# Performance work log

Hardware: AMD Instinct MI355X
Metric: run time of the kernel (lower is better)

Reference implementation:

```python
import jax, jax.numpy as jnp
import numpy as np

SIDE = 32
N_NODES = SIDE * SIDE          # n_nodes = 1024
WIDTH = 128
IN_DIM = 128
T_DIM = 2
U_DIM = 1
BATCH = 8
MSG_STEPS = int(np.sqrt(N_NODES))  # 32
LN_EPS = 1e-5


def _create_grid():
    # matches GEN.create_grid for t_dim == 2
    pos = np.array([[i / (SIDE - 1), j / (SIDE - 1)]
                    for i in range(SIDE) for j in range(SIDE)], dtype=np.float32)
    edges = []
    for i in range(1, SIDE):
        for j in range(1, SIDE):
            a = SIDE * i + j
            b = SIDE * (i - 1) + j
            c = SIDE * i + (j - 1)
            edges += [[a, b], [b, a], [c, a], [a, c]]
    edge_index = np.array(edges, dtype=np.int64).T  # [2, E]
    return pos, edge_index


def setup_inputs() -> dict:
    key = jax.random.key(0)
    ks = jax.random.split(key, 16)
    node_pos_np, edge_index_np = _create_grid()

    def lin(k, fan_in, fan_out):
        kw, kb = jax.random.split(k)
        bound = 1.0 / np.sqrt(fan_in)
        W = jax.random.uniform(kw, (fan_in, fan_out), jnp.float32, -bound, bound)
        b = jax.random.uniform(kb, (fan_out,), jnp.float32, -bound, bound)
        return W, b

    We1, be1 = lin(ks[0], IN_DIM, WIDTH)
    We2, be2 = lin(ks[1], WIDTH, WIDTH)
    We3, be3 = lin(ks[2], WIDTH, WIDTH)
    Wg, bg = lin(ks[3], WIDTH + T_DIM, WIDTH)
    Wd1, bd1 = lin(ks[4], WIDTH + T_DIM, WIDTH)
    Wd2, bd2 = lin(ks[5], WIDTH, WIDTH)
    Wd3, bd3 = lin(ks[6], WIDTH, U_DIM)

    return {
        'X1': jax.random.uniform(ks[7], (BATCH, IN_DIM + T_DIM), jnp.float32),
        'node_pos': jnp.asarray(node_pos_np),
        'edge_index': jnp.asarray(edge_index_np),
        'We1': We1, 'be1': be1, 'We2': We2, 'be2': be2, 'We3': We3, 'be3': be3,
        'Wg': Wg, 'bg': bg,
        'gamma': jnp.ones((WIDTH,), jnp.float32),
        'beta': jnp.zeros((WIDTH,), jnp.float32),
        'Wd1': Wd1, 'bd1': bd1, 'Wd2': Wd2, 'bd2': bd2, 'Wd3': Wd3, 'bd3': bd3,
    }


def _gen_forward(X1, node_pos, edge_index, We1, be1, We2, be2, We3, be3,
                 Wg, bg, gamma, beta, Wd1, bd1, Wd2, bd2, Wd3, bd3):
    s, t = X1[:, :-T_DIM], X1[:, -T_DIM:]

    # encoder MLP: Linear-ReLU-Linear-ReLU-Linear
    h = jax.nn.relu(s @ We1 + be1)
    h = jax.nn.relu(h @ We2 + be2)
    enc = h @ We3 + be3                                   # [B, W]

    # per-sample graph construction: softmax over node distance to origin
    # (identical for every sample), node_features = weight @ enc[i][None,:]
    d0 = jnp.sqrt(jnp.sum(node_pos ** 2, axis=1, keepdims=True))  # [N,1]
    w0 = jax.nn.softmax(-d0, axis=0)                              # [N,1]
    x = w0[None, :, :] * enc[:, None, :]                          # [B,N,W]

    # GCNConv normalization with added self-loops (symmetric norm)
    row, col = edge_index[0], edge_index[1]
    deg = jnp.ones((N_NODES,), x.dtype).at[col].add(1.0)
    dinv = deg ** -0.5
    enorm = dinv[row] * dinv[col]   # edge norm
    snorm = dinv * dinv             # self-loop norm
    posb = jnp.broadcast_to(node_pos[None], (x.shape[0], N_NODES, T_DIM))

    def step(xc, _):
        xin = jnp.concatenate([posb, xc], axis=-1)        # [B,N,W+2]
        xw = xin @ Wg                                     # [B,N,W]
        msgs = enorm[None, :, None] * xw[:, row, :]       # [B,E,W]
        agg = (snorm[None, :, None] * xw).at[:, col, :].add(msgs) + bg
        xn = xc + agg
        mu = jnp.mean(xn, axis=-1, keepdims=True)
        var = jnp.var(xn, axis=-1, keepdims=True)
        xn = (xn - mu) * jax.lax.rsqrt(var + LN_EPS) * gamma + beta
        return xn, None

    x, _ = jax.lax.scan(step, x, None, length=MSG_STEPS)  # [B,N,W]

    # readout: softmax over node distance to query point t
    dist = jnp.sqrt(jnp.sum((node_pos[None] - t[:, None, :]) ** 2,
                            axis=2, keepdims=True))       # [B,N,1]
    wt = jax.nn.softmax(-dist, axis=1)                    # [B,N,1]
    hidden = jnp.einsum('bnk,bnw->bw', wt, x)             # [B,W]
    hidden = jnp.concatenate([hidden, t], axis=1)

    h = jax.nn.relu(hidden @ Wd1 + bd1)
    h = jax.nn.relu(h @ Wd2 + bd2)
    y = (h @ Wd3 + bd3).squeeze()                         # [B] (u_dim == 1)
    return y


def reference(X1, node_pos, edge_index, We1, be1, We2, be2, We3, be3,
              Wg, bg, gamma, beta, Wd1, bd1, Wd2, bd2, Wd3, bd3):
    return _gen_forward(X1, node_pos, edge_index, We1, be1, We2, be2, We3, be3,
                        Wg, bg, gamma, beta, Wd1, bd1, Wd2, bd2, Wd3, bd3)
```

## Files before the change

### kernel.cpp

```cpp
#include <hip/hip_runtime.h>

#define NODES 1024
#define WD    128
#define NSTEPS 32
#define LNEPS 1e-5f

typedef __bf16 bf16x8 __attribute__((ext_vector_type(8)));
typedef float  f32x4  __attribute__((ext_vector_type(4)));
typedef int    i32x4  __attribute__((ext_vector_type(4)));

__device__ __forceinline__ f32x4 mfma16(i32x4 a, i32x4 b, f32x4 c) {
  return __builtin_amdgcn_mfma_f32_16x16x32_bf16(
      __builtin_bit_cast(bf16x8, a), __builtin_bit_cast(bf16x8, b), c, 0, 0, 0);
}

__device__ __forceinline__ unsigned short f2bf(float f) {
  union { float f; unsigned u; } v; v.f = f;
  unsigned r = v.u + 0x7FFF + ((v.u >> 16) & 1);
  return (unsigned short)(r >> 16);
}
__device__ __forceinline__ float bf2f(unsigned short h) {
  union { unsigned u; float f; } v; v.u = ((unsigned)h) << 16;
  return v.f;
}

__device__ __forceinline__ float dinv_of(int n) {
  const int i = n >> 5, j = n & 31;
  int cnt = 1;
  cnt += (i >= 1 && j >= 1) ? 1 : 0;
  cnt += (i <= 30 && j >= 1) ? 1 : 0;
  cnt += (i >= 1 && j >= 1) ? 1 : 0;
  cnt += (i >= 1 && j <= 30) ? 1 : 0;
  return 1.f / sqrtf((float)cnt);
}

__device__ void enc_layer(const float* __restrict__ W,
                          const float* __restrict__ bias,
                          const float* __restrict__ src, float* __restrict__ dst,
                          float* __restrict__ Wst, int tid, int b, int c,
                          bool relu_) {
  float acc = bias ? bias[c] : 0.f;
  for (int h = 0; h < 2; h++) {
    __syncthreads();
    for (int i = tid; i < 2048; i += 1024)
      ((float4*)Wst)[i] = ((const float4*)(W + h * 8192))[i];
    __syncthreads();
#pragma unroll 8
    for (int k = 0; k < 64; k++)
      acc += src[b * WD + 64 * h + k] * Wst[k * WD + c];
  }
  __syncthreads();
  dst[tid] = relu_ ? fmaxf(acc, 0.f) : acc;
}

__global__ __launch_bounds__(1024) void setup_kernel(
    const float* __restrict__ X1, const float* __restrict__ pos,
    const float* __restrict__ We1, const float* __restrict__ be1,
    const float* __restrict__ We2, const float* __restrict__ be2,
    const float* __restrict__ We3, const float* __restrict__ be3,
    const float* __restrict__ Wg,
    float* __restrict__ enc_out, float* __restrict__ E2,
    float* __restrict__ w0sum, int* __restrict__ Bpk) {
  __shared__ float Wst[64 * WD];
  __shared__ float ioA[1024];
  __shared__ float ioB[1024];
  const int tid = threadIdx.x;
  const int b = tid >> 7, c = tid & 127;
  ioA[tid] = X1[b * 130 + c];
  enc_layer(We1, be1, ioA, ioB, Wst, tid, b, c, true);
  enc_layer(We2, be2, ioB, ioA, Wst, tid, b, c, true);
  enc_layer(We3, be3, ioA, ioB, Wst, tid, b, c, false);
  enc_out[tid] = ioB[tid];
  const float* W2 = Wg + 2 * WD;
  {
    float acc = 0.f;
    for (int h = 0; h < 2; h++) {
      __syncthreads();
      for (int i = tid; i < 2048; i += 1024)
        ((float4*)Wst)[i] = ((const float4*)(W2 + h * 8192))[i];
      __syncthreads();
#pragma unroll 8
      for (int k = 0; k < 64; k++)
        acc += ioB[b * WD + 64 * h + k] * Wst[k * WD + c];
    }
    E2[tid] = acc;
  }
  __syncthreads();
  {
    const float px = pos[2 * tid], py = pos[2 * tid + 1];
    ioA[tid] = expf(-sqrtf(px * px + py * py));
  }
  __syncthreads();
  for (int s = 512; s > 0; s >>= 1) {
    if (tid < s) ioA[tid] += ioA[tid + s];
    __syncthreads();
  }
  if (tid == 0) w0sum[0] = ioA[0];
  if (tid < 512) {
    const int nt = tid >> 6, l = tid & 63;
    const int g8 = (l >> 4) << 3;
    const int n = 16 * nt + (l & 15);
    const int base = (nt * 64 + l) * 32;
#pragma unroll
    for (int kt = 0; kt < 4; kt++) {
#pragma unroll
      for (int d = 0; d < 4; d++) {
        const int k0 = 32 * kt + g8 + 2 * d;
        const float w0_ = W2[k0 * WD + n];
        const float w1_ = W2[(k0 + 1) * WD + n];
        const unsigned short h0 = f2bf(w0_), h1 = f2bf(w1_);
        const unsigned short l0 = f2bf(w0_ - bf2f(h0)), l1 = f2bf(w1_ - bf2f(h1));
        Bpk[base + kt * 4 + d] = (int)h0 | ((int)h1 << 16);
        Bpk[base + 16 + kt * 4 + d] = (int)l0 | ((int)l1 << 16);
      }
    }
  }
}

__global__ __launch_bounds__(256) void init_kernel(
    const float* __restrict__ pos, const float* __restrict__ Wg,
    const float* __restrict__ bg, const float* __restrict__ enc,
    const float* __restrict__ E2, const float* __restrict__ w0sum,
    float* __restrict__ X, float* __restrict__ XW0, float* __restrict__ Q) {
  const int tid = threadIdx.x;
  const int v0 = blockIdx.x * 4;
  const int lr = tid >> 3, cq = tid & 7, c0 = cq * 16;
  const int b = lr >> 2, nl = lr & 3, v = v0 + nl;
  const int grow = (b << 10) + v;
  const float px = pos[2 * v], py = pos[2 * v + 1];
  const float w0v = expf(-sqrtf(px * px + py * py)) / w0sum[0];
#pragma unroll
  for (int q4 = 0; q4 < 4; q4++) {
    const float4 e = *(const float4*)(enc + b * WD + c0 + 4 * q4);
    const float4 e2 = *(const float4*)(E2 + b * WD + c0 + 4 * q4);
    *(float4*)(X + (size_t)grow * WD + c0 + 4 * q4) =
        make_float4(w0v * e.x, w0v * e.y, w0v * e.z, w0v * e.w);
    *(float4*)(XW0 + (size_t)grow * WD + c0 + 4 * q4) =
        make_float4(w0v * e2.x, w0v * e2.y, w0v * e2.z, w0v * e2.w);
  }
  for (int i = tid; i < 512; i += 256) {
    const int vq = v0 + (i >> 7);
    const int cc = i & 127;
    const float dv = dinv_of(vq);
    const float dvv = dv * dv;
    const int iv = vq >> 5, jv = vq & 31;
    float cx = dvv * pos[2 * vq], cy = dvv * pos[2 * vq + 1];
    const bool ex[4] = {(iv >= 1) && (jv >= 1), (iv <= 30) && (jv >= 1),
                        (iv >= 1) && (jv >= 1), (iv >= 1) && (jv <= 30)};
    const int du[4] = {-32, 32, -1, 1};
#pragma unroll
    for (int e = 0; e < 4; e++) {
      if (ex[e]) {
        const int u = vq + du[e];
        const float w = dinv_of(u) * dv;
        cx += w * pos[2 * u];
        cy += w * pos[2 * u + 1];
      }
    }
    Q[vq * WD + cc] = bg[cc] + cx * Wg[cc] + cy * Wg[WD + cc];
  }
}

__global__ __launch_bounds__(256) void step_kernel(
    float* __restrict__ X, const float* __restrict__ XWin,
    float* __restrict__ XWout, const int* __restrict__ Bpk,
    const float* __restrict__ Q, const float* __restrict__ gamma,
    const float* __restrict__ beta, const int mode) {
  __shared__ int Ah[32 * 65];
  __shared__ int Al[32 * 65];
  const int tid = threadIdx.x;
  const int v0 = blockIdx.x * 4;

  const int lr = tid >> 3, cq = tid & 7, c0 = cq * 16;
  const int b = lr >> 2, nl = lr & 3, v = v0 + nl;
  const int grow = (b << 10) + v;
  const float dv = dinv_of(v);
  const float dvv = dv * dv;
  const int iv = v >> 5, jv = v & 31;
  const bool ex[4] = {(iv >= 1) && (jv >= 1), (iv <= 30) && (jv >= 1),
                      (iv >= 1) && (jv >= 1), (iv >= 1) && (jv <= 30)};
  const int du[4] = {-32, 32, -1, 1};

  float y[16];
  {
    const float* xr = X + (size_t)grow * WD + c0;
    const float* qr = Q + v * WD + c0;
    const float* wr = XWin + (size_t)grow * WD + c0;
#pragma unroll
    for (int q4 = 0; q4 < 4; q4++) {
      const float4 a = *(const float4*)(xr + 4 * q4);
      const float4 qq = *(const float4*)(qr + 4 * q4);
      const float4 w = *(const float4*)(wr + 4 * q4);
      y[4 * q4 + 0] = a.x + qq.x + dvv * w.x;
      y[4 * q4 + 1] = a.y + qq.y + dvv * w.y;
      y[4 * q4 + 2] = a.z + qq.z + dvv * w.z;
      y[4 * q4 + 3] = a.w + qq.w + dvv * w.w;
    }
  }
#pragma unroll
  for (int e = 0; e < 4; e++) {
    const int u = ex[e] ? v + du[e] : v;
    const float w = ex[e] ? dinv_of(u) * dv : 0.f;
    const float* nr = XWin + (size_t)((b << 10) + u) * WD + c0;
#pragma unroll
    for (int q4 = 0; q4 < 4; q4++) {
      const float4 t = *(const float4*)(nr + 4 * q4);
      y[4 * q4 + 0] += w * t.x;
      y[4 * q4 + 1] += w * t.y;
      y[4 * q4 + 2] += w * t.z;
      y[4 * q4 + 3] += w * t.w;
    }
  }
  float s1 = 0.f, s2 = 0.f;
#pragma unroll
  for (int q = 0; q < 16; q++) { s1 += y[q]; s2 += y[q] * y[q]; }
#pragma unroll
  for (int m = 1; m < 8; m <<= 1) {
    s1 += __shfl_xor(s1, m);
    s2 += __shfl_xor(s2, m);
  }
  const float mu = s1 * (1.f / 128.f);
  const float var = s2 * (1.f / 128.f) - mu * mu;
  const float rs = 1.f / sqrtf(var + LNEPS);
  {
    const float* g4 = gamma + c0;
    const float* b4 = beta + c0;
    float* xo = X + (size_t)grow * WD + c0;
    int hw[8], lw[8];
#pragma unroll
    for (int d = 0; d < 8; d++) {
      const float xa = (y[2 * d] - mu) * rs * g4[2 * d] + b4[2 * d];
      const float xb = (y[2 * d + 1] - mu) * rs * g4[2 * d + 1] + b4[2 * d + 1];
      *(float2*)(xo + 2 * d) = make_float2(xa, xb);
      const unsigned short ha = f2bf(xa), hb = f2bf(xb);
      hw[d] = (int)ha | ((int)hb << 16);
      lw[d] = (int)f2bf(xa - bf2f(ha)) | ((int)f2bf(xb - bf2f(hb)) << 16);
    }
    const int abase = lr * 65 + cq * 8;
    *(i32x4*)(Ah + abase) = i32x4{hw[0], hw[1], hw[2], hw[3]};
    *(i32x4*)(Ah + abase + 4) = i32x4{hw[4], hw[5], hw[6], hw[7]};
    *(i32x4*)(Al + abase) = i32x4{lw[0], lw[1], lw[2], lw[3]};
    *(i32x4*)(Al + abase + 4) = i32x4{lw[4], lw[5], lw[6], lw[7]};
  }
  __syncthreads();

  if (mode) {
    const int l = tid & 63, w = tid >> 6;
    const int g4 = (l >> 4) << 2;
    const int mrow0 = (l & 15) * 65;
    const int mrow1 = mrow0 + 16 * 65;
    i32x4 bh[2][4], bl[2][4];
    {
      const int lb0 = (2 * w * 64 + l) * 32;
#pragma unroll
      for (int ntl = 0; ntl < 2; ntl++)
#pragma unroll
        for (int kt = 0; kt < 4; kt++) {
          bh[ntl][kt] = *(const i32x4*)(Bpk + lb0 + ntl * 2048 + kt * 4);
          bl[ntl][kt] = *(const i32x4*)(Bpk + lb0 + ntl * 2048 + 16 + kt * 4);
        }
    }
    f32x4 acc[2][2] = {};
#pragma unroll
    for (int kt = 0; kt < 4; kt++) {
      const int off = 16 * kt + g4;
      const i32x4 ah0 = *(const i32x4*)(Ah + mrow0 + off);
      const i32x4 ah1 = *(const i32x4*)(Ah + mrow1 + off);
      const i32x4 al0 = *(const i32x4*)(Al + mrow0 + off);
      const i32x4 al1 = *(const i32x4*)(Al + mrow1 + off);
#pragma unroll
      for (int ntl = 0; ntl < 2; ntl++) {
        acc[0][ntl] = mfma16(ah0, bh[ntl][kt], acc[0][ntl]);
        acc[1][ntl] = mfma16(ah1, bh[ntl][kt], acc[1][ntl]);
        acc[0][ntl] = mfma16(ah0, bl[ntl][kt], acc[0][ntl]);
        acc[1][ntl] = mfma16(ah1, bl[ntl][kt], acc[1][ntl]);
        acc[0][ntl] = mfma16(al0, bh[ntl][kt], acc[0][ntl]);
        acc[1][ntl] = mfma16(al1, bh[ntl][kt], acc[1][ntl]);
      }
    }
    const int colbase = 32 * w + (l & 15);
    const int rbase = (l >> 4) << 2;
#pragma unroll
    for (int mt = 0; mt < 2; mt++)
#pragma unroll
      for (int ntl = 0; ntl < 2; ntl++)
#pragma unroll
        for (int r = 0; r < 4; r++) {
          const int lrr = 16 * mt + rbase + r;
          const int gr = ((lrr >> 2) << 10) + v0 + (lrr & 3);
          XWout[(size_t)gr * WD + colbase + 16 * ntl] = acc[mt][ntl][r];
        }
  }
}

__global__ __launch_bounds__(1024) void hid_kernel(
    const float* __restrict__ pos, const float* __restrict__ X1,
    const float* __restrict__ Xout, float* __restrict__ hidden) {
  __shared__ float wsh[NODES];
  __shared__ float red[16];
  __shared__ float asum[8][WD];
  const int b = blockIdx.x;
  const int n = threadIdx.x;
  const float tx = X1[b * 130 + 128], ty = X1[b * 130 + 129];
  const float px = pos[2 * n] - tx, py = pos[2 * n + 1] - ty;
  const float e = expf(-sqrtf(px * px + py * py));
  float s = e;
#pragma unroll
  for (int m = 32; m >= 1; m >>= 1) s += __shfl_xor(s, m);
  if ((n & 63) == 0) red[n >> 6] = s;
  __syncthreads();
  float tot = 0.f;
#pragma unroll
  for (int w = 0; w < 16; w++) tot += red[w];
  wsh[n] = e / tot;
  __syncthreads();
  const int c = n & 127, g = n >> 7;
  const float* xp = Xout + ((size_t)b * NODES + g * 128) * WD + c;
  const float* wp = wsh + g * 128;
  float a = 0.f;
#pragma unroll 4
  for (int it = 0; it < 128; it++) a += wp[it] * xp[it * WD];
  asum[g][c] = a;
  __syncthreads();
  if (g == 0) {
    float t2 = a;
#pragma unroll
    for (int gg = 1; gg < 8; gg++) t2 += asum[gg][c];
    hidden[b * 130 + c] = t2;
  }
  if (n == 0) {
    hidden[b * 130 + 128] = tx;
    hidden[b * 130 + 129] = ty;
  }
}

__global__ __launch_bounds__(128) void dec_kernel(
    const float* __restrict__ hidden, const float* __restrict__ Wd1,
    const float* __restrict__ bd1, const float* __restrict__ Wd2,
    const float* __restrict__ bd2, const float* __restrict__ Wd3,
    const float* __restrict__ bd3, float* __restrict__ out) {
  __shared__ float hin[130];
  __shared__ float hh[WD];
  __shared__ float red2[2];
  const int b = blockIdx.x;
  const int c = threadIdx.x;
  for (int idx = c; idx < 130; idx += 128) hin[idx] = hidden[b * 130 + idx];
  __syncthreads();
  float a0 = bd1[c], a1 = 0.f;
#pragma unroll 8
  for (int k = 0; k < 130; k += 2) {
    a0 += hin[k] * Wd1[k * WD + c];
    a1 += hin[k + 1] * Wd1[(k + 1) * WD + c];
  }
  hh[c] = fmaxf(a0 + a1, 0.f);
  __syncthreads();
  a0 = bd2[c];
  a1 = 0.f;
#pragma unroll 8
  for (int k = 0; k < WD; k += 2) {
    a0 += hh[k] * Wd2[k * WD + c];
    a1 += hh[k + 1] * Wd2[(k + 1) * WD + c];
  }
  const float h2v = fmaxf(a0 + a1, 0.f);
  float p = h2v * Wd3[c];
#pragma unroll
  for (int m = 32; m >= 1; m >>= 1) p += __shfl_xor(p, m);
  if ((c & 63) == 0) red2[c >> 6] = p;
  __syncthreads();
  if (c == 0) out[b] = red2[0] + red2[1] + bd3[0];
}

extern "C" void kernel_launch(void* const* d_in, const int* in_sizes, int n_in,
                              void* d_out, int out_size, void* d_ws,
                              size_t ws_size, hipStream_t stream) {
  const float* X1 = (const float*)d_in[0];
  const float* pos = (const float*)d_in[1];
  const float* We1 = (const float*)d_in[3];
  const float* be1 = (const float*)d_in[4];
  const float* We2 = (const float*)d_in[5];
  const float* be2 = (const float*)d_in[6];
  const float* We3 = (const float*)d_in[7];
  const float* be3 = (const float*)d_in[8];
  const float* Wg = (const float*)d_in[9];
  const float* bg = (const float*)d_in[10];
  const float* gamma = (const float*)d_in[11];
  const float* beta = (const float*)d_in[12];
  const float* Wd1 = (const float*)d_in[13];
  const float* bd1 = (const float*)d_in[14];
  const float* Wd2 = (const float*)d_in[15];
  const float* bd2 = (const float*)d_in[16];
  const float* Wd3 = (const float*)d_in[17];
  const float* bd3 = (const float*)d_in[18];
  float* out = (float*)d_out;
  float* f = (float*)d_ws;

  float* w0sum = f;
  float* enc = f + 16;
  float* E2 = f + 1056;
  float* hidden = f + 2096;
  float* Q = f + 4096;
  int* Bpk = (int*)(f + 135168);
  float* X = f + 151552;
  float* XWa = f + 1200128;
  float* XWb = f + 2248704;

  setup_kernel<<<1, 1024, 0, stream>>>(X1, pos, We1, be1, We2, be2, We3, be3,
                                       Wg, enc, E2, w0sum, Bpk);
  init_kernel<<<256, 256, 0, stream>>>(pos, Wg, bg, enc, E2, w0sum, X, XWa, Q);
  for (int t = 0; t < NSTEPS; t++) {
    const float* xin = (t & 1) ? XWb : XWa;
    float* xout = (t & 1) ? XWa : XWb;
    step_kernel<<<256, 256, 0, stream>>>(X, xin, xout, Bpk, Q, gamma, beta,
                                         (t < NSTEPS - 1) ? 1 : 0);
  }
  hid_kernel<<<8, 1024, 0, stream>>>(pos, X1, X, hidden);
  dec_kernel<<<8, 128, 0, stream>>>(hidden, Wd1, bd1, Wd2, bd2, Wd3, bd3, out);
  (void)in_sizes;
  (void)n_in;
  (void)out_size;
  (void)ws_size;
}
```

Measured before the change: 303.5 us.

## Fuse setup into init, widen step blocks to 512 threads, merge readout and decoder

The single-block setup kernel is folded into the init kernel. Every block now recomputes the encoder MLP and the softmax normaliser redundantly, and each block writes a slice of the packed bf16 weights. The step kernel goes to 512 threads, with one 16-column MFMA tile per wave instead of two, and it preloads the B fragments before the aggregation phase. The hidden and decoder kernels are merged, which cuts launches from 36 to 34 and removes a serial 1-block setup stage, at the cost of redundant encoder work across 256 blocks.

```diff
diff --git a/kernel.cpp b/kernel.cpp
--- a/kernel.cpp
+++ b/kernel.cpp
@@ -34,113 +34,84 @@
   return 1.f / sqrtf((float)cnt);
 }
 
-__device__ void enc_layer(const float* __restrict__ W,
-                          const float* __restrict__ bias,
-                          const float* __restrict__ src, float* __restrict__ dst,
-                          float* __restrict__ Wst, int tid, int b, int c,
-                          bool relu_) {
-  float acc = bias ? bias[c] : 0.f;
-  for (int h = 0; h < 2; h++) {
-    __syncthreads();
-    for (int i = tid; i < 2048; i += 1024)
-      ((float4*)Wst)[i] = ((const float4*)(W + h * 8192))[i];
-    __syncthreads();
+__device__ __forceinline__ void lay512(const float* __restrict__ W,
+                                       const float* __restrict__ bias,
+                                       const float* __restrict__ src,
+                                       float* __restrict__ dst, int tid,
+                                       bool relu_) {
+  const int c = tid & 127;
+  const int b0 = tid >> 7;
+  float a0 = bias ? bias[c] : 0.f;
+  float a1 = a0;
 #pragma unroll 8
-    for (int k = 0; k < 64; k++)
-      acc += src[b * WD + 64 * h + k] * Wst[k * WD + c];
-  }
-  __syncthreads();
-  dst[tid] = relu_ ? fmaxf(acc, 0.f) : acc;
-}
-
-__global__ __launch_bounds__(1024) void setup_kernel(
+  for (int k = 0; k < WD; k++) {
+    const float wv = W[k * WD + c];
+    a0 += src[b0 * WD + k] * wv;
+    a1 += src[(b0 + 4) * WD + k] * wv;
+  }
+  dst[b0 * WD + c] = relu_ ? fmaxf(a0, 0.f) : a0;
+  dst[(b0 + 4) * WD + c] = relu_ ? fmaxf(a1, 0.f) : a1;
+  __syncthreads();
+}
+
+__global__ __launch_bounds__(512) void init_kernel(
     const float* __restrict__ X1, const float* __restrict__ pos,
     const float* __restrict__ We1, const float* __restrict__ be1,
     const float* __restrict__ We2, const float* __restrict__ be2,
     const float* __restrict__ We3, const float* __restrict__ be3,
-    const float* __restrict__ Wg,
-    float* __restrict__ enc_out, float* __restrict__ E2,
-    float* __restrict__ w0sum, int* __restrict__ Bpk) {
-  __shared__ float Wst[64 * WD];
+    const float* __restrict__ Wg, const float* __restrict__ bg,
+    float* __restrict__ X, float* __restrict__ XW0, float* __restrict__ Q,
+    int* __restrict__ Bpk) {
   __shared__ float ioA[1024];
   __shared__ float ioB[1024];
-  const int tid = threadIdx.x;
-  const int b = tid >> 7, c = tid & 127;
-  ioA[tid] = X1[b * 130 + c];
-  enc_layer(We1, be1, ioA, ioB, Wst, tid, b, c, true);
-  enc_layer(We2, be2, ioB, ioA, Wst, tid, b, c, true);
-  enc_layer(We3, be3, ioA, ioB, Wst, tid, b, c, false);
-  enc_out[tid] = ioB[tid];
-  const float* W2 = Wg + 2 * WD;
-  {
-    float acc = 0.f;
-    for (int h = 0; h < 2; h++) {
-      __syncthreads();
-      for (int i = tid; i < 2048; i += 1024)
-        ((float4*)Wst)[i] = ((const float4*)(W2 + h * 8192))[i];
-      __syncthreads();
-#pragma unroll 8
-      for (int k = 0; k < 64; k++)
-        acc += ioB[b * WD + 64 * h + k] * Wst[k * WD + c];
-    }
-    E2[tid] = acc;
-  }
-  __syncthreads();
-  {
-    const float px = pos[2 * tid], py = pos[2 * tid + 1];
-    ioA[tid] = expf(-sqrtf(px * px + py * py));
-  }
-  __syncthreads();
-  for (int s = 512; s > 0; s >>= 1) {
-    if (tid < s) ioA[tid] += ioA[tid + s];
-    __syncthreads();
-  }
-  if (tid == 0) w0sum[0] = ioA[0];
-  if (tid < 512) {
-    const int nt = tid >> 6, l = tid & 63;
-    const int g8 = (l >> 4) << 3;
-    const int n = 16 * nt + (l & 15);
-    const int base = (nt * 64 + l) * 32;
-#pragma unroll
-    for (int kt = 0; kt < 4; kt++) {
-#pragma unroll
-      for (int d = 0; d < 4; d++) {
-        const int k0 = 32 * kt + g8 + 2 * d;
-        const float w0_ = W2[k0 * WD + n];
-        const float w1_ = W2[(k0 + 1) * WD + n];
-        const unsigned short h0 = f2bf(w0_), h1 = f2bf(w1_);
-        const unsigned short l0 = f2bf(w0_ - bf2f(h0)), l1 = f2bf(w1_ - bf2f(h1));
-        Bpk[base + kt * 4 + d] = (int)h0 | ((int)h1 << 16);
-        Bpk[base + 16 + kt * 4 + d] = (int)l0 | ((int)l1 << 16);
-      }
-    }
-  }
-}
-
-__global__ __launch_bounds__(256) void init_kernel(
-    const float* __restrict__ pos, const float* __restrict__ Wg,
-    const float* __restrict__ bg, const float* __restrict__ enc,
-    const float* __restrict__ E2, const float* __restrict__ w0sum,
-    float* __restrict__ X, float* __restrict__ XW0, float* __restrict__ Q) {
+  __shared__ float red[512];
   const int tid = threadIdx.x;
   const int v0 = blockIdx.x * 4;
-  const int lr = tid >> 3, cq = tid & 7, c0 = cq * 16;
-  const int b = lr >> 2, nl = lr & 3, v = v0 + nl;
-  const int grow = (b << 10) + v;
-  const float px = pos[2 * v], py = pos[2 * v + 1];
-  const float w0v = expf(-sqrtf(px * px + py * py)) / w0sum[0];
-#pragma unroll
-  for (int q4 = 0; q4 < 4; q4++) {
-    const float4 e = *(const float4*)(enc + b * WD + c0 + 4 * q4);
-    const float4 e2 = *(const float4*)(E2 + b * WD + c0 + 4 * q4);
-    *(float4*)(X + (size_t)grow * WD + c0 + 4 * q4) =
-        make_float4(w0v * e.x, w0v * e.y, w0v * e.z, w0v * e.w);
-    *(float4*)(XW0 + (size_t)grow * WD + c0 + 4 * q4) =
-        make_float4(w0v * e2.x, w0v * e2.y, w0v * e2.z, w0v * e2.w);
-  }
-  for (int i = tid; i < 512; i += 256) {
-    const int vq = v0 + (i >> 7);
-    const int cc = i & 127;
+  const float* W2 = Wg + 2 * WD;
+
+  for (int i = tid; i < 1024; i += 512) ioA[i] = X1[(i >> 7) * 130 + (i & 127)];
+  __syncthreads();
+  lay512(We1, be1, ioA, ioB, tid, true);
+  lay512(We2, be2, ioB, ioA, tid, true);
+  lay512(We3, be3, ioA, ioB, tid, false);
+  lay512(W2, nullptr, ioB, ioA, tid, false);
+
+  {
+    float es = 0.f;
+#pragma unroll
+    for (int r = 0; r < 2; r++) {
+      const int n = tid + 512 * r;
+      const float px = pos[2 * n], py = pos[2 * n + 1];
+      es += expf(-sqrtf(px * px + py * py));
+    }
+    red[tid] = es;
+  }
+  __syncthreads();
+  for (int s = 256; s > 0; s >>= 1) {
+    if (tid < s) red[tid] += red[tid + s];
+    __syncthreads();
+  }
+  const float w0sum = red[0];
+
+  {
+    const int lr = tid >> 4, cq = tid & 15, c0 = cq * 8;
+    const int b = lr >> 2, nl = lr & 3, v = v0 + nl;
+    const int grow = (b << 10) + v;
+    const float pxv = pos[2 * v], pyv = pos[2 * v + 1];
+    const float w0v = expf(-sqrtf(pxv * pxv + pyv * pyv)) / w0sum;
+#pragma unroll
+    for (int q4 = 0; q4 < 2; q4++) {
+      const float4 e = *(const float4*)(ioB + b * WD + c0 + 4 * q4);
+      const float4 e2 = *(const float4*)(ioA + b * WD + c0 + 4 * q4);
+      *(float4*)(X + (size_t)grow * WD + c0 + 4 * q4) =
+          make_float4(w0v * e.x, w0v * e.y, w0v * e.z, w0v * e.w);
+      *(float4*)(XW0 + (size_t)grow * WD + c0 + 4 * q4) =
+          make_float4(w0v * e2.x, w0v * e2.y, w0v * e2.z, w0v * e2.w);
+    }
+  }
+  {
+    const int vq = v0 + (tid >> 7);
+    const int cc = tid & 127;
     const float dv = dinv_of(vq);
     const float dvv = dv * dv;
     const int iv = vq >> 5, jv = vq & 31;
@@ -159,19 +130,47 @@
     }
     Q[vq * WD + cc] = bg[cc] + cx * Wg[cc] + cy * Wg[WD + cc];
   }
-}
-
-__global__ __launch_bounds__(256) void step_kernel(
+  if (tid < 64) {
+    const int e = blockIdx.x * 64 + tid;
+    const int nt = e >> 11, l = (e >> 5) & 63, half = (e >> 4) & 1;
+    const int kt = (e >> 2) & 3, d = e & 3;
+    const int k0 = 32 * kt + ((l >> 4) << 3) + 2 * d;
+    const int n = 16 * nt + (l & 15);
+    const float w0_ = W2[k0 * WD + n];
+    const float w1_ = W2[(k0 + 1) * WD + n];
+    const unsigned short h0 = f2bf(w0_), h1 = f2bf(w1_);
+    int val;
+    if (half == 0) {
+      val = (int)h0 | ((int)h1 << 16);
+    } else {
+      val = (int)f2bf(w0_ - bf2f(h0)) | ((int)f2bf(w1_ - bf2f(h1)) << 16);
+    }
+    Bpk[e] = val;
+  }
+}
+
+__global__ __launch_bounds__(512) void step_kernel(
     float* __restrict__ X, const float* __restrict__ XWin,
     float* __restrict__ XWout, const int* __restrict__ Bpk,
     const float* __restrict__ Q, const float* __restrict__ gamma,
     const float* __restrict__ beta, const int mode) {
-  __shared__ int Ah[32 * 65];
-  __shared__ int Al[32 * 65];
+  __shared__ int Ah[32 * 68];
+  __shared__ int Al[32 * 68];
   const int tid = threadIdx.x;
   const int v0 = blockIdx.x * 4;
-
-  const int lr = tid >> 3, cq = tid & 7, c0 = cq * 16;
+  const int wv = tid >> 6, l = tid & 63;
+
+  i32x4 bh[4], bl[4];
+  if (mode) {
+    const int lb0 = (wv * 64 + l) * 32;
+#pragma unroll
+    for (int kt = 0; kt < 4; kt++) {
+      bh[kt] = *(const i32x4*)(Bpk + lb0 + kt * 4);
+      bl[kt] = *(const i32x4*)(Bpk + lb0 + 16 + kt * 4);
+    }
+  }
+
+  const int lr = tid >> 4, cq = tid & 15, c0 = cq * 8;
   const int b = lr >> 2, nl = lr & 3, v = v0 + nl;
   const int grow = (b << 10) + v;
   const float dv = dinv_of(v);
@@ -181,13 +180,13 @@
                       (iv >= 1) && (jv >= 1), (iv >= 1) && (jv <= 30)};
   const int du[4] = {-32, 32, -1, 1};
 
-  float y[16];
+  float y[8];
   {
     const float* xr = X + (size_t)grow * WD + c0;
     const float* qr = Q + v * WD + c0;
     const float* wr = XWin + (size_t)grow * WD + c0;
 #pragma unroll
-    for (int q4 = 0; q4 < 4; q4++) {
+    for (int q4 = 0; q4 < 2; q4++) {
       const float4 a = *(const float4*)(xr + 4 * q4);
       const float4 qq = *(const float4*)(qr + 4 * q4);
       const float4 w = *(const float4*)(wr + 4 * q4);
@@ -203,7 +202,7 @@
     const float w = ex[e] ? dinv_of(u) * dv : 0.f;
     const float* nr = XWin + (size_t)((b << 10) + u) * WD + c0;
 #pragma unroll
-    for (int q4 = 0; q4 < 4; q4++) {
+    for (int q4 = 0; q4 < 2; q4++) {
       const float4 t = *(const float4*)(nr + 4 * q4);
       y[4 * q4 + 0] += w * t.x;
       y[4 * q4 + 1] += w * t.y;
@@ -213,9 +212,9 @@
   }
   float s1 = 0.f, s2 = 0.f;
 #pragma unroll
-  for (int q = 0; q < 16; q++) { s1 += y[q]; s2 += y[q] * y[q]; }
-#pragma unroll
-  for (int m = 1; m < 8; m <<= 1) {
+  for (int q = 0; q < 8; q++) { s1 += y[q]; s2 += y[q] * y[q]; }
+#pragma unroll
+  for (int m = 1; m < 16; m <<= 1) {
     s1 += __shfl_xor(s1, m);
     s2 += __shfl_xor(s2, m);
   }
@@ -226,41 +225,33 @@
     const float* g4 = gamma + c0;
     const float* b4 = beta + c0;
     float* xo = X + (size_t)grow * WD + c0;
-    int hw[8], lw[8];
-#pragma unroll
-    for (int d = 0; d < 8; d++) {
-      const float xa = (y[2 * d] - mu) * rs * g4[2 * d] + b4[2 * d];
-      const float xb = (y[2 * d + 1] - mu) * rs * g4[2 * d + 1] + b4[2 * d + 1];
-      *(float2*)(xo + 2 * d) = make_float2(xa, xb);
-      const unsigned short ha = f2bf(xa), hb = f2bf(xb);
-      hw[d] = (int)ha | ((int)hb << 16);
-      lw[d] = (int)f2bf(xa - bf2f(ha)) | ((int)f2bf(xb - bf2f(hb)) << 16);
-    }
-    const int abase = lr * 65 + cq * 8;
-    *(i32x4*)(Ah + abase) = i32x4{hw[0], hw[1], hw[2], hw[3]};
-    *(i32x4*)(Ah + abase + 4) = i32x4{hw[4], hw[5], hw[6], hw[7]};
-    *(i32x4*)(Al + abase) = i32x4{lw[0], lw[1], lw[2], lw[3]};
-    *(i32x4*)(Al + abase + 4) = i32x4{lw[4], lw[5], lw[6], lw[7]};
-  }
-  __syncthreads();
+    float xn[8];
+#pragma unroll
+    for (int q = 0; q < 8; q++) xn[q] = (y[q] - mu) * rs * g4[q] + b4[q];
+    *(float4*)(xo) = make_float4(xn[0], xn[1], xn[2], xn[3]);
+    *(float4*)(xo + 4) = make_float4(xn[4], xn[5], xn[6], xn[7]);
+    if (mode) {
+      int hw[4], lw[4];
+#pragma unroll
+      for (int d = 0; d < 4; d++) {
+        const unsigned short ha = f2bf(xn[2 * d]);
+        const unsigned short hb = f2bf(xn[2 * d + 1]);
+        hw[d] = (int)ha | ((int)hb << 16);
+        lw[d] = (int)f2bf(xn[2 * d] - bf2f(ha)) |
+                ((int)f2bf(xn[2 * d + 1] - bf2f(hb)) << 16);
+      }
+      const int abase = lr * 68 + cq * 4;
+      *(i32x4*)(Ah + abase) = i32x4{hw[0], hw[1], hw[2], hw[3]};
+      *(i32x4*)(Al + abase) = i32x4{lw[0], lw[1], lw[2], lw[3]};
+    }
+  }
 
   if (mode) {
-    const int l = tid & 63, w = tid >> 6;
+    __syncthreads();
     const int g4 = (l >> 4) << 2;
-    const int mrow0 = (l & 15) * 65;
-    const int mrow1 = mrow0 + 16 * 65;
-    i32x4 bh[2][4], bl[2][4];
-    {
-      const int lb0 = (2 * w * 64 + l) * 32;
-#pragma unroll
-      for (int ntl = 0; ntl < 2; ntl++)
-#pragma unroll
-        for (int kt = 0; kt < 4; kt++) {
-          bh[ntl][kt] = *(const i32x4*)(Bpk + lb0 + ntl * 2048 + kt * 4);
-          bl[ntl][kt] = *(const i32x4*)(Bpk + lb0 + ntl * 2048 + 16 + kt * 4);
-        }
-    }
-    f32x4 acc[2][2] = {};
+    const int mrow0 = (l & 15) * 68;
+    const int mrow1 = mrow0 + 16 * 68;
+    f32x4 acc[2] = {};
 #pragma unroll
     for (int kt = 0; kt < 4; kt++) {
       const int off = 16 * kt + g4;
@@ -268,37 +259,37 @@
       const i32x4 ah1 = *(const i32x4*)(Ah + mrow1 + off);
       const i32x4 al0 = *(const i32x4*)(Al + mrow0 + off);
       const i32x4 al1 = *(const i32x4*)(Al + mrow1 + off);
-#pragma unroll
-      for (int ntl = 0; ntl < 2; ntl++) {
-        acc[0][ntl] = mfma16(ah0, bh[ntl][kt], acc[0][ntl]);
-        acc[1][ntl] = mfma16(ah1, bh[ntl][kt], acc[1][ntl]);
-        acc[0][ntl] = mfma16(ah0, bl[ntl][kt], acc[0][ntl]);
-        acc[1][ntl] = mfma16(ah1, bl[ntl][kt], acc[1][ntl]);
-        acc[0][ntl] = mfma16(al0, bh[ntl][kt], acc[0][ntl]);
-        acc[1][ntl] = mfma16(al1, bh[ntl][kt], acc[1][ntl]);
+      acc[0] = mfma16(ah0, bh[kt], acc[0]);
+      acc[1] = mfma16(ah1, bh[kt], acc[1]);
+      acc[0] = mfma16(ah0, bl[kt], acc[0]);
+      acc[1] = mfma16(ah1, bl[kt], acc[1]);
+      acc[0] = mfma16(al0, bh[kt], acc[0]);
+      acc[1] = mfma16(al1, bh[kt], acc[1]);
+    }
+    const int colb = 16 * wv + (l & 15);
+    const int rbase = (l >> 4) << 2;
+#pragma unroll
+    for (int mt = 0; mt < 2; mt++)
+#pragma unroll
+      for (int r = 0; r < 4; r++) {
+        const int lrr = 16 * mt + rbase + r;
+        const int gr = ((lrr >> 2) << 10) + v0 + (lrr & 3);
+        XWout[(size_t)gr * WD + colb] = acc[mt][r];
       }
-    }
-    const int colbase = 32 * w + (l & 15);
-    const int rbase = (l >> 4) << 2;
-#pragma unroll
-    for (int mt = 0; mt < 2; mt++)
-#pragma unroll
-      for (int ntl = 0; ntl < 2; ntl++)
-#pragma unroll
-        for (int r = 0; r < 4; r++) {
-          const int lrr = 16 * mt + rbase + r;
-          const int gr = ((lrr >> 2) << 10) + v0 + (lrr & 3);
-          XWout[(size_t)gr * WD + colbase + 16 * ntl] = acc[mt][ntl][r];
-        }
-  }
-}
-
-__global__ __launch_bounds__(1024) void hid_kernel(
+  }
+}
+
+__global__ __launch_bounds__(1024) void hiddec_kernel(
     const float* __restrict__ pos, const float* __restrict__ X1,
-    const float* __restrict__ Xout, float* __restrict__ hidden) {
+    const float* __restrict__ Xf, const float* __restrict__ Wd1,
+    const float* __restrict__ bd1, const float* __restrict__ Wd2,
+    const float* __restrict__ bd2, const float* __restrict__ Wd3,
+    const float* __restrict__ bd3, float* __restrict__ out) {
   __shared__ float wsh[NODES];
   __shared__ float red[16];
   __shared__ float asum[8][WD];
+  __shared__ float hid[132];
+  __shared__ float hh[WD];
   const int b = blockIdx.x;
   const int n = threadIdx.x;
   const float tx = X1[b * 130 + 128], ty = X1[b * 130 + 129];
@@ -315,59 +306,43 @@
   wsh[n] = e / tot;
   __syncthreads();
   const int c = n & 127, g = n >> 7;
-  const float* xp = Xout + ((size_t)b * NODES + g * 128) * WD + c;
-  const float* wp = wsh + g * 128;
-  float a = 0.f;
+  {
+    const float* xp = Xf + ((size_t)b * NODES + g * 128) * WD + c;
+    const float* wp = wsh + g * 128;
+    float a = 0.f;
 #pragma unroll 4
-  for (int it = 0; it < 128; it++) a += wp[it] * xp[it * WD];
-  asum[g][c] = a;
+    for (int it = 0; it < 128; it++) a += wp[it] * xp[it * WD];
+    asum[g][c] = a;
+  }
   __syncthreads();
   if (g == 0) {
-    float t2 = a;
+    float t2 = asum[0][c];
 #pragma unroll
     for (int gg = 1; gg < 8; gg++) t2 += asum[gg][c];
-    hidden[b * 130 + c] = t2;
-  }
-  if (n == 0) {
-    hidden[b * 130 + 128] = tx;
-    hidden[b * 130 + 129] = ty;
-  }
-}
-
-__global__ __launch_bounds__(128) void dec_kernel(
-    const float* __restrict__ hidden, const float* __restrict__ Wd1,
-    const float* __restrict__ bd1, const float* __restrict__ Wd2,
-    const float* __restrict__ bd2, const float* __restrict__ Wd3,
-    const float* __restrict__ bd3, float* __restrict__ out) {
-  __shared__ float hin[130];
-  __shared__ float hh[WD];
-  __shared__ float red2[2];
-  const int b = blockIdx.x;
-  const int c = threadIdx.x;
-  for (int idx = c; idx < 130; idx += 128) hin[idx] = hidden[b * 130 + idx];
-  __syncthreads();
-  float a0 = bd1[c], a1 = 0.f;
+    hid[c] = t2;
+  }
+  if (n == 0) { hid[128] = tx; hid[129] = ty; }
+  __syncthreads();
+  float a1v = 0.f;
+  if (n < 128) {
+    a1v = bd1[n];
+    for (int k = 0; k < 130; k++) a1v += hid[k] * Wd1[k * WD + n];
+  }
+  __syncthreads();
+  if (n < 128) hh[n] = fmaxf(a1v, 0.f);
+  __syncthreads();
+  float p = 0.f;
+  if (n < 128) {
+    float a2 = bd2[n];
 #pragma unroll 8
-  for (int k = 0; k < 130; k += 2) {
-    a0 += hin[k] * Wd1[k * WD + c];
-    a1 += hin[k + 1] * Wd1[(k + 1) * WD + c];
-  }
-  hh[c] = fmaxf(a0 + a1, 0.f);
-  __syncthreads();
-  a0 = bd2[c];
-  a1 = 0.f;
-#pragma unroll 8
-  for (int k = 0; k < WD; k += 2) {
-    a0 += hh[k] * Wd2[k * WD + c];
-    a1 += hh[k + 1] * Wd2[(k + 1) * WD + c];
-  }
-  const float h2v = fmaxf(a0 + a1, 0.f);
-  float p = h2v * Wd3[c];
+    for (int k = 0; k < WD; k++) a2 += hh[k] * Wd2[k * WD + n];
+    p = fmaxf(a2, 0.f) * Wd3[n];
+  }
 #pragma unroll
   for (int m = 32; m >= 1; m >>= 1) p += __shfl_xor(p, m);
-  if ((c & 63) == 0) red2[c >> 6] = p;
-  __syncthreads();
-  if (c == 0) out[b] = red2[0] + red2[1] + bd3[0];
+  if ((n & 63) == 0) red[n >> 6] = p;
+  __syncthreads();
+  if (n == 0) out[b] = red[0] + red[1] + bd3[0];
 }
 
 extern "C" void kernel_launch(void* const* d_in, const int* in_sizes, int n_in,
@@ -394,27 +369,22 @@
   float* out = (float*)d_out;
   float* f = (float*)d_ws;
 
-  float* w0sum = f;
-  float* enc = f + 16;
-  float* E2 = f + 1056;
-  float* hidden = f + 2096;
-  float* Q = f + 4096;
-  int* Bpk = (int*)(f + 135168);
-  float* X = f + 151552;
-  float* XWa = f + 1200128;
-  float* XWb = f + 2248704;
-
-  setup_kernel<<<1, 1024, 0, stream>>>(X1, pos, We1, be1, We2, be2, We3, be3,
-                                       Wg, enc, E2, w0sum, Bpk);
-  init_kernel<<<256, 256, 0, stream>>>(pos, Wg, bg, enc, E2, w0sum, X, XWa, Q);
+  float* Q = f;
+  int* Bpk = (int*)(f + 131072);
+  float* X = f + 147456;
+  float* XWa = f + 1196032;
+  float* XWb = f + 2244608;
+
+  init_kernel<<<256, 512, 0, stream>>>(X1, pos, We1, be1, We2, be2, We3, be3,
+                                       Wg, bg, X, XWa, Q, Bpk);
   for (int t = 0; t < NSTEPS; t++) {
     const float* xin = (t & 1) ? XWb : XWa;
     float* xout = (t & 1) ? XWa : XWb;
-    step_kernel<<<256, 256, 0, stream>>>(X, xin, xout, Bpk, Q, gamma, beta,
+    step_kernel<<<256, 512, 0, stream>>>(X, xin, xout, Bpk, Q, gamma, beta,
                                          (t < NSTEPS - 1) ? 1 : 0);
   }
-  hid_kernel<<<8, 1024, 0, stream>>>(pos, X1, X, hidden);
-  dec_kernel<<<8, 128, 0, stream>>>(hidden, Wd1, bd1, Wd2, bd2, Wd3, bd3, out);
+  hiddec_kernel<<<8, 1024, 0, stream>>>(pos, X1, X, Wd1, bd1, Wd2, bd2, Wd3,
+                                        bd3, out);
   (void)in_sizes;
   (void)n_in;
   (void)out_size;
```

Measured after the change: 263.8 us, median of 2. -13.1%, faster.
